# Kernel tuning notes

Hardware: AMD Instinct MI355X
Metric: run time of the kernel (lower is better)

## Reference

```python
import jax, jax.numpy as jnp
import numpy as np

STATE_DIM = 1024
ACTION_DIM = 512
TASK_DIM = 64
EMBED = 64
HID = 128
B = 256


def setup_inputs() -> dict:
    key = jax.random.key(0)
    ks = jax.random.split(key, 24)
    s = 0.02
    inp = {
        "obs": jax.random.normal(ks[0], (B, STATE_DIM), dtype=jnp.float32),
        "task_label": jax.random.normal(ks[1], (B, TASK_DIM), dtype=jnp.float32),
        "action": jax.random.randint(ks[2], (B,), 0, ACTION_DIM, dtype=jnp.int64 if jax.config.jax_enable_x64 else jnp.int32),
        # task encoder: Linear(64,64) ReLU Linear(64,64) ReLU
        "we1": jax.random.normal(ks[3], (TASK_DIM, EMBED)) * s,
        "be1": jnp.zeros((EMBED,), jnp.float32),
        "we2": jax.random.normal(ks[4], (EMBED, EMBED)) * s,
        "be2": jnp.zeros((EMBED,), jnp.float32),
        # h_action net_W: Linear(64,128) ReLU Linear(128, 512*1024)
        "aw1": jax.random.normal(ks[5], (EMBED, HID)) * s,
        "aw1b": jnp.zeros((HID,), jnp.float32),
        "aw2": jax.random.normal(ks[6], (HID, ACTION_DIM * STATE_DIM)) * s,
        "aw2b": jnp.zeros((ACTION_DIM * STATE_DIM,), jnp.float32),
        # h_action net_b: Linear(64,128) ReLU Linear(128, 512)
        "ab1": jax.random.normal(ks[7], (EMBED, HID)) * s,
        "ab1b": jnp.zeros((HID,), jnp.float32),
        "ab2": jax.random.normal(ks[8], (HID, ACTION_DIM)) * s,
        "ab2b": jnp.zeros((ACTION_DIM,), jnp.float32),
        # h_critic net_W: Linear(64,128) ReLU Linear(128, 1*1024)
        "cw1": jax.random.normal(ks[9], (EMBED, HID)) * s,
        "cw1b": jnp.zeros((HID,), jnp.float32),
        "cw2": jax.random.normal(ks[10], (HID, 1 * STATE_DIM)) * s,
        "cw2b": jnp.zeros((STATE_DIM,), jnp.float32),
        # h_critic net_b: Linear(64,128) ReLU Linear(128, 1)
        "cb1": jax.random.normal(ks[11], (EMBED, HID)) * s,
        "cb1b": jnp.zeros((HID,), jnp.float32),
        "cb2": jax.random.normal(ks[12], (HID, 1)) * s,
        "cb2b": jnp.zeros((1,), jnp.float32),
    }
    return inp


def reference(obs, task_label, action, we1, be1, we2, be2,
              aw1, aw1b, aw2, aw2b, ab1, ab1b, ab2, ab2b,
              cw1, cw1b, cw2, cw2b, cb1, cb1b, cb2, cb2b):
    relu = jax.nn.relu
    b = obs.shape[0]
    # DummyBody: phi = phi_a = phi_v = obs
    # task encoder -> z [B, EMBED]
    z = relu(relu(task_label @ we1 + be1) @ we2 + be2)
    # hypernet-generated actor head: W [B, A, S], b [B, A]
    Wa = (relu(z @ aw1 + aw1b) @ aw2 + aw2b).reshape(b, ACTION_DIM, STATE_DIM)
    ba = relu(z @ ab1 + ab1b) @ ab2 + ab2b
    # hypernet-generated critic head: W [B, 1, S], b [B, 1]
    Wv = (relu(z @ cw1 + cw1b) @ cw2 + cw2b).reshape(b, 1, STATE_DIM)
    bv = relu(z @ cb1 + cb1b) @ cb2 + cb2b
    # bmm apply (torch.bmm(W, phi.unsqueeze(-1)).squeeze(-1) + b)
    logits = jnp.einsum('boi,bi->bo', Wa, obs) + ba
    v = jnp.einsum('boi,bi->bo', Wv, obs) + bv
    logp = jax.nn.log_softmax(logits, axis=-1)
    log_prob = jnp.take_along_axis(logp, action[:, None].astype(jnp.int32), axis=-1)  # [B,1]
    entropy = -jnp.sum(jnp.exp(logp) * logp, axis=-1, keepdims=True)  # [B,1]
    return logits, action, log_prob, entropy, v
```

## Files before the change

kernel.cpp:

```cpp
#include <hip/hip_runtime.h>
#include <hip/hip_bf16.h>

#define B_SZ 256
#define SDIM 1024
#define ADIM 512

#define BK 128
#define KSPLIT 2
#define KHALF (SDIM / KSPLIT)
#define NCHUNK (KHALF / BK)
#define ROWS 80
#define PADB 136
#define NSLOT 10

typedef __attribute__((ext_vector_type(8))) short bf16x8;
typedef __attribute__((ext_vector_type(4))) float f32x4;

__device__ __forceinline__ unsigned short f2bf(float x) {
  union { float f; unsigned u; } v; v.f = x;
  unsigned r = v.u + 0x7FFFu + ((v.u >> 16) & 1u);
  return (unsigned short)(r >> 16);
}

__global__ __launch_bounds__(128) void kprep(
    const float* __restrict__ obs,
    const float* __restrict__ task, const int* __restrict__ action,
    const float* __restrict__ we1, const float* __restrict__ be1,
    const float* __restrict__ we2, const float* __restrict__ be2,
    const float* __restrict__ aw1, const float* __restrict__ aw1b,
    const float* __restrict__ ab1, const float* __restrict__ ab1b,
    const float* __restrict__ ab2, const float* __restrict__ ab2b,
    const float* __restrict__ cw1, const float* __restrict__ cw1b,
    const float* __restrict__ cb1, const float* __restrict__ cb1b,
    const float* __restrict__ cb2, const float* __restrict__ cb2b,
    float* __restrict__ ws_ha, float* __restrict__ ws_hc,
    unsigned short* __restrict__ ws_obs,
    float* __restrict__ out)
{
  const int b = blockIdx.x, t = threadIdx.x;
  __shared__ float s_task[64], s_t1[64], s_z[64], s_hb[128], s_red[128];

  {
    const float4* orow = (const float4*)(obs + (size_t)b * SDIM);
    ushort4* wrow = (ushort4*)(ws_obs + (size_t)b * SDIM);
#pragma unroll
    for (int i = 0; i < 2; ++i) {
      const int idx = t + i * 128;
      float4 v = orow[idx];
      ushort4 u;
      u.x = f2bf(v.x); u.y = f2bf(v.y); u.z = f2bf(v.z); u.w = f2bf(v.w);
      wrow[idx] = u;
    }
  }

  if (t < 64) s_task[t] = task[b * 64 + t];
  __syncthreads();
  if (t < 64) {
    float a = be1[t];
    for (int e = 0; e < 64; ++e) a += s_task[e] * we1[e * 64 + t];
    s_t1[t] = fmaxf(a, 0.0f);
  }
  __syncthreads();
  if (t < 64) {
    float a = be2[t];
    for (int e = 0; e < 64; ++e) a += s_t1[e] * we2[e * 64 + t];
    s_z[t] = fmaxf(a, 0.0f);
  }
  __syncthreads();
  {
    float a1 = aw1b[t], a2 = ab1b[t], a3 = cw1b[t], a4 = cb1b[t];
    for (int e = 0; e < 64; ++e) {
      const float zv = s_z[e];
      a1 += zv * aw1[e * 128 + t];
      a2 += zv * ab1[e * 128 + t];
      a3 += zv * cw1[e * 128 + t];
      a4 += zv * cb1[e * 128 + t];
    }
    ws_ha[b * 128 + t] = fmaxf(a1, 0.0f);
    s_hb[t] = fmaxf(a2, 0.0f);
    ws_hc[b * 128 + t] = fmaxf(a3, 0.0f);
    s_red[t] = fmaxf(a4, 0.0f) * cb2[t];
  }
  __syncthreads();
  for (int o = t; o < ADIM; o += 128) {
    float a = ab2b[o];
    for (int h = 0; h < 128; ++h) a += s_hb[h] * ab2[h * ADIM + o];
    out[b * ADIM + o] = a;
  }
  for (int s = 64; s > 0; s >>= 1) {
    __syncthreads();
    if (t < s) s_red[t] += s_red[t + s];
  }
  if (t == 0) {
    out[131840 + b] = s_red[0] + cb2b[0];
    out[131072 + b] = (float)action[b];
  }
}

__global__ __launch_bounds__(256, 2) void khyper(
    const unsigned short* __restrict__ ws_obs,
    const float* __restrict__ aw2, const float* __restrict__ aw2b,
    const float* __restrict__ cw2, const float* __restrict__ cw2b,
    const float* __restrict__ ws_ha, const float* __restrict__ ws_hc,
    float* __restrict__ d_out)
{
  __shared__ unsigned short B_lds[ROWS * PADB];
  __shared__ float logits_buf[B_SZ];

  const int tid = threadIdx.x;
  const int blk = blockIdx.x;
  const int kh   = blk & 1;
  const int half = (blk >> 1) & 1;
  const int col  = blk >> 2;
  const bool critic = (col == ADIM);
  const float* haW = critic ? ws_hc : ws_ha;
  const float* Wbase = critic ? cw2 : (aw2 + (size_t)col * SDIM);
  const size_t wstride = critic ? (size_t)SDIM : (size_t)ADIM * SDIM;
  const float* Bbias = critic ? cw2b : (aw2b + (size_t)col * SDIM);
  const int kbase = kh * KHALF;

  const int lr0 = tid >> 5;
  const int c4  = tid & 31;
  const int g0  = half * ROWS + lr0;
  const float* src0 = Wbase + (size_t)g0 * wstride + c4 * 4 + kbase;
  const size_t off8 = (size_t)8 * wstride;
  const float* biassrc = Bbias + c4 * 4 + kbase;
  const int soff0 = lr0 * PADB + c4 * 4;

  const int lane = tid & 63;
  const int wv = tid >> 6;
  const int mbase = wv * 64;
  const int lrow = lane & 15;
  const int lk8 = (lane >> 4) * 8;

  const unsigned short* pA[4];
#pragma unroll
  for (int mf = 0; mf < 4; ++mf)
    pA[mf] = ws_obs + (size_t)(mbase + mf * 16 + lrow) * SDIM + kbase + lk8;

  f32x4 acc[4][5];
#pragma unroll
  for (int mf = 0; mf < 4; ++mf)
#pragma unroll
    for (int nf = 0; nf < 5; ++nf) acc[mf][nf] = (f32x4)(0.0f);

  float4 sreg[NSLOT];

  auto LOAD = [&](int c) {
    const int k0 = c * BK;
#pragma unroll
    for (int i = 0; i < NSLOT; ++i) {
      const int g = g0 + 8 * i;
      float4 v; v.x = 0.f; v.y = 0.f; v.z = 0.f; v.w = 0.f;
      if (g < 128)       v = *(const float4*)(src0 + (size_t)i * off8 + k0);
      else if (g == 128) v = *(const float4*)(biassrc + k0);
      sreg[i] = v;
    }
  };

  auto WRITE = [&]() {
#pragma unroll
    for (int i = 0; i < NSLOT; ++i) {
      ushort4 p;
      p.x = f2bf(sreg[i].x); p.y = f2bf(sreg[i].y);
      p.z = f2bf(sreg[i].z); p.w = f2bf(sreg[i].w);
      *(ushort4*)(&B_lds[soff0 + i * 8 * PADB]) = p;
    }
  };

  auto COMPUTE = [&](int c) {
    const int kg = c * BK;
#pragma unroll
    for (int kk = 0; kk < BK / 32; ++kk) {
      bf16x8 af[4];
#pragma unroll
      for (int mf = 0; mf < 4; ++mf)
        af[mf] = *(const bf16x8*)(pA[mf] + kg + kk * 32);
      bf16x8 bfr[5];
#pragma unroll
      for (int nf = 0; nf < 5; ++nf)
        bfr[nf] = *(const bf16x8*)(&B_lds[(nf * 16 + lrow) * PADB + kk * 32 + lk8]);
#pragma unroll
      for (int mf = 0; mf < 4; ++mf)
#pragma unroll
        for (int nf = 0; nf < 5; ++nf)
          acc[mf][nf] = __builtin_amdgcn_mfma_f32_16x16x32_bf16(af[mf], bfr[nf], acc[mf][nf], 0, 0, 0);
    }
  };

  const int rot = blk & 3;
  LOAD(rot);
#pragma unroll 1
  for (int c = 0; c < NCHUNK; ++c) {
    const int ce = (c + rot) & 3;
    WRITE();
    asm volatile("s_waitcnt lgkmcnt(0)" ::: "memory");
    __builtin_amdgcn_sched_barrier(0);
    __builtin_amdgcn_s_barrier();
    if (c + 1 < NCHUNK) LOAD((c + 1 + rot) & 3);
    COMPUTE(ce);
    __builtin_amdgcn_sched_barrier(0);
    __builtin_amdgcn_s_barrier();
  }

  if (tid < B_SZ) logits_buf[tid] = 0.0f;
  __syncthreads();

  float val[4][4];
#pragma unroll
  for (int mf = 0; mf < 4; ++mf)
#pragma unroll
    for (int r = 0; r < 4; ++r) val[mf][r] = 0.0f;

#pragma unroll
  for (int nf = 0; nf < 5; ++nf) {
    const int hidx = half * ROWS + nf * 16 + lrow;
    if (hidx < 128) {
#pragma unroll
      for (int mf = 0; mf < 4; ++mf) {
        const int m0 = mbase + mf * 16 + ((lane >> 4) << 2);
#pragma unroll
        for (int r = 0; r < 4; ++r)
          val[mf][r] += haW[(m0 + r) * 128 + hidx] * acc[mf][nf][r];
      }
    } else if (hidx == 128) {
#pragma unroll
      for (int mf = 0; mf < 4; ++mf)
#pragma unroll
        for (int r = 0; r < 4; ++r) val[mf][r] += acc[mf][nf][r];
    }
  }

#pragma unroll
  for (int mf = 0; mf < 4; ++mf)
#pragma unroll
    for (int r = 0; r < 4; ++r) {
      float v = val[mf][r];
      v += __shfl_xor(v, 1, 64);
      v += __shfl_xor(v, 2, 64);
      v += __shfl_xor(v, 4, 64);
      v += __shfl_xor(v, 8, 64);
      val[mf][r] = v;
    }
  if ((lane & 15) == 0) {
#pragma unroll
    for (int mf = 0; mf < 4; ++mf)
#pragma unroll
      for (int r = 0; r < 4; ++r)
        atomicAdd(&logits_buf[mbase + mf * 16 + ((lane >> 4) << 2) + r], val[mf][r]);
  }
  __syncthreads();

  if (tid < B_SZ) {
    if (!critic) atomicAdd(&d_out[(size_t)tid * ADIM + col], logits_buf[tid]);
    else         atomicAdd(&d_out[131840 + tid], logits_buf[tid]);
  }
}

__global__ __launch_bounds__(256) void kfinal(const int* __restrict__ action,
                                              float* __restrict__ d_out)
{
  const int b = blockIdx.x, t = threadIdx.x;
  const float* lrow = d_out + (size_t)b * ADIM;
  __shared__ float sM[4], sS[4], sT[4];

  const float x0 = lrow[t], x1 = lrow[t + 256];
  float m = fmaxf(x0, x1);
#pragma unroll
  for (int s = 1; s < 64; s <<= 1) m = fmaxf(m, __shfl_xor(m, s, 64));
  const int wv = t >> 6, ln = t & 63;
  if (ln == 0) sM[wv] = m;
  __syncthreads();
  m = fmaxf(fmaxf(sM[0], sM[1]), fmaxf(sM[2], sM[3]));

  const float d0 = x0 - m, d1 = x1 - m;
  const float e0 = expf(d0), e1 = expf(d1);
  float s1 = e0 + e1;
  float s2 = e0 * d0 + e1 * d1;
#pragma unroll
  for (int s = 1; s < 64; s <<= 1) {
    s1 += __shfl_xor(s1, s, 64);
    s2 += __shfl_xor(s2, s, 64);
  }
  if (ln == 0) { sS[wv] = s1; sT[wv] = s2; }
  __syncthreads();
  if (t == 0) {
    const float S = sS[0] + sS[1] + sS[2] + sS[3];
    const float T = sT[0] + sT[1] + sT[2] + sT[3];
    const float lnS = logf(S);
    const int a = action[b];
    d_out[131328 + b] = (lrow[a] - m) - lnS;
    d_out[131584 + b] = lnS - T / S;
  }
}

extern "C" void kernel_launch(void* const* d_in, const int* in_sizes, int n_in,
                              void* d_out_v, int out_size, void* d_ws, size_t ws_size,
                              hipStream_t stream) {
  const float* obs   = (const float*)d_in[0];
  const float* task  = (const float*)d_in[1];
  const int*   action= (const int*)  d_in[2];
  const float* we1   = (const float*)d_in[3];
  const float* be1   = (const float*)d_in[4];
  const float* we2   = (const float*)d_in[5];
  const float* be2   = (const float*)d_in[6];
  const float* aw1   = (const float*)d_in[7];
  const float* aw1b  = (const float*)d_in[8];
  const float* aw2   = (const float*)d_in[9];
  const float* aw2b  = (const float*)d_in[10];
  const float* ab1   = (const float*)d_in[11];
  const float* ab1b  = (const float*)d_in[12];
  const float* ab2   = (const float*)d_in[13];
  const float* ab2b  = (const float*)d_in[14];
  const float* cw1   = (const float*)d_in[15];
  const float* cw1b  = (const float*)d_in[16];
  const float* cw2   = (const float*)d_in[17];
  const float* cw2b  = (const float*)d_in[18];
  const float* cb1   = (const float*)d_in[19];
  const float* cb1b  = (const float*)d_in[20];
  const float* cb2   = (const float*)d_in[21];
  const float* cb2b  = (const float*)d_in[22];
  float* out = (float*)d_out_v;
  float* ws_ha = (float*)d_ws;
  float* ws_hc = ws_ha + 256 * 128;
  unsigned short* ws_obs = (unsigned short*)(ws_hc + 256 * 128);

  kprep<<<256, 128, 0, stream>>>(obs, task, action, we1, be1, we2, be2, aw1, aw1b,
                                 ab1, ab1b, ab2, ab2b, cw1, cw1b, cb1, cb1b,
                                 cb2, cb2b, ws_ha, ws_hc, ws_obs, out);
  khyper<<<513 * 4, 256, 0, stream>>>(ws_obs, aw2, aw2b, cw2, cw2b, ws_ha, ws_hc, out);
  kfinal<<<256, 256, 0, stream>>>(action, out);
}
```

Before: 166.6 us.

## Restructure hypernet GEMM to tile over output/hidden with full-batch MFMA per block

Replaces the per-column, K-split hypernet kernel with 552 blocks of 512 threads. Each block streams 16-output by 128-k weight tiles for 8 hidden units and multiplies them against all 256 batch rows. It scales each tile's result by the hidden activation and accumulates in registers, with double-buffered swizzled LDS. The critic bias term cw2b·obs moves into the prep kernel, so the hyper kernel no longer carries a bias row. This aims to cut redundant obs reloads, the shared-memory reduction and atomic traffic. In exchange, each block has few loads in flight and a barrier every step, and 16 hidden groups contend on the output atomics.

```diff
diff --git a/kernel.cpp b/kernel.cpp
--- a/kernel.cpp
+++ b/kernel.cpp
@@ -5,13 +5,8 @@
 #define SDIM 1024
 #define ADIM 512
 
-#define BK 128
-#define KSPLIT 2
-#define KHALF (SDIM / KSPLIT)
-#define NCHUNK (KHALF / BK)
-#define ROWS 80
-#define PADB 136
-#define NSLOT 10
+#define BKC 128
+#define NKC (SDIM / BKC)
 
 typedef __attribute__((ext_vector_type(8))) short bf16x8;
 typedef __attribute__((ext_vector_type(4))) float f32x4;
@@ -33,6 +28,7 @@
     const float* __restrict__ cw1, const float* __restrict__ cw1b,
     const float* __restrict__ cb1, const float* __restrict__ cb1b,
     const float* __restrict__ cb2, const float* __restrict__ cb2b,
+    const float* __restrict__ cw2b,
     float* __restrict__ ws_ha, float* __restrict__ ws_hc,
     unsigned short* __restrict__ ws_obs,
     float* __restrict__ out)
@@ -40,13 +36,17 @@
   const int b = blockIdx.x, t = threadIdx.x;
   __shared__ float s_task[64], s_t1[64], s_z[64], s_hb[128], s_red[128];
 
+  float dotc = 0.0f;
   {
     const float4* orow = (const float4*)(obs + (size_t)b * SDIM);
+    const float4* crow = (const float4*)cw2b;
     ushort4* wrow = (ushort4*)(ws_obs + (size_t)b * SDIM);
 #pragma unroll
     for (int i = 0; i < 2; ++i) {
       const int idx = t + i * 128;
       float4 v = orow[idx];
+      float4 w = crow[idx];
+      dotc += v.x * w.x + v.y * w.y + v.z * w.z + v.w * w.w;
       ushort4 u;
       u.x = f2bf(v.x); u.y = f2bf(v.y); u.z = f2bf(v.z); u.w = f2bf(v.w);
       wrow[idx] = u;
@@ -79,7 +79,7 @@
     ws_ha[b * 128 + t] = fmaxf(a1, 0.0f);
     s_hb[t] = fmaxf(a2, 0.0f);
     ws_hc[b * 128 + t] = fmaxf(a3, 0.0f);
-    s_red[t] = fmaxf(a4, 0.0f) * cb2[t];
+    s_red[t] = fmaxf(a4, 0.0f) * cb2[t] + dotc;
   }
   __syncthreads();
   for (int o = t; o < ADIM; o += 128) {
@@ -97,163 +97,142 @@
   }
 }
 
-__global__ __launch_bounds__(256, 2) void khyper(
+__global__ __launch_bounds__(512, 4) void khyper(
     const unsigned short* __restrict__ ws_obs,
     const float* __restrict__ aw2, const float* __restrict__ aw2b,
-    const float* __restrict__ cw2, const float* __restrict__ cw2b,
+    const float* __restrict__ cw2,
     const float* __restrict__ ws_ha, const float* __restrict__ ws_hc,
     float* __restrict__ d_out)
 {
-  __shared__ unsigned short B_lds[ROWS * PADB];
-  __shared__ float logits_buf[B_SZ];
+  __shared__ unsigned short Wl[2][16 * BKC];
 
   const int tid = threadIdx.x;
   const int blk = blockIdx.x;
-  const int kh   = blk & 1;
-  const int half = (blk >> 1) & 1;
-  const int col  = blk >> 2;
-  const bool critic = (col == ADIM);
-  const float* haW = critic ? ws_hc : ws_ha;
-  const float* Wbase = critic ? cw2 : (aw2 + (size_t)col * SDIM);
-  const size_t wstride = critic ? (size_t)SDIM : (size_t)ADIM * SDIM;
-  const float* Bbias = critic ? cw2b : (aw2b + (size_t)col * SDIM);
-  const int kbase = kh * KHALF;
-
-  const int lr0 = tid >> 5;
-  const int c4  = tid & 31;
-  const int g0  = half * ROWS + lr0;
-  const float* src0 = Wbase + (size_t)g0 * wstride + c4 * 4 + kbase;
-  const size_t off8 = (size_t)8 * wstride;
-  const float* biassrc = Bbias + c4 * 4 + kbase;
-  const int soff0 = lr0 * PADB + c4 * 4;
+
+  int wtype, o0 = 0, h0 = 0, hcount;
+  const float* Wbase;
+  size_t hstride = 0;
+  if (blk < 512) {
+    wtype = 0; o0 = (blk & 31) * 16; h0 = (blk >> 5) * 8; hcount = 8;
+    Wbase = aw2 + ((size_t)h0 * ADIM + o0) * SDIM;
+    hstride = (size_t)ADIM * SDIM;
+  } else if (blk < 544) {
+    wtype = 1; o0 = (blk - 512) * 16; hcount = 1;
+    Wbase = aw2b + (size_t)o0 * SDIM;
+  } else {
+    wtype = 2; hcount = 1;
+    Wbase = cw2 + (size_t)(blk - 544) * 16 * SDIM;
+  }
+  const int steps = NKC * hcount;
+
+  const int sr = tid >> 5;
+  const int sc = tid & 31;
+  const float* wsrc = Wbase + (size_t)sr * SDIM + sc * 4;
+  const int wldsb = ((sr * 256 + sc * 8) ^ ((sr & 7) << 4));
 
   const int lane = tid & 63;
   const int wv = tid >> 6;
-  const int mbase = wv * 64;
   const int lrow = lane & 15;
-  const int lk8 = (lane >> 4) * 8;
-
-  const unsigned short* pA[4];
-#pragma unroll
-  for (int mf = 0; mf < 4; ++mf)
-    pA[mf] = ws_obs + (size_t)(mbase + mf * 16 + lrow) * SDIM + kbase + lk8;
-
-  f32x4 acc[4][5];
-#pragma unroll
-  for (int mf = 0; mf < 4; ++mf)
-#pragma unroll
-    for (int nf = 0; nf < 5; ++nf) acc[mf][nf] = (f32x4)(0.0f);
-
-  float4 sreg[NSLOT];
-
-  auto LOAD = [&](int c) {
-    const int k0 = c * BK;
-#pragma unroll
-    for (int i = 0; i < NSLOT; ++i) {
-      const int g = g0 + 8 * i;
-      float4 v; v.x = 0.f; v.y = 0.f; v.z = 0.f; v.w = 0.f;
-      if (g < 128)       v = *(const float4*)(src0 + (size_t)i * off8 + k0);
-      else if (g == 128) v = *(const float4*)(biassrc + k0);
-      sreg[i] = v;
-    }
+  const int grp = lane >> 4;
+
+  const int b0 = wv * 32 + lrow;
+  const int b1 = wv * 32 + 16 + lrow;
+
+  int ardb[4];
+#pragma unroll
+  for (int ks = 0; ks < 4; ++ks)
+    ardb[ks] = ((lrow * 256 + ks * 64 + grp * 16) ^ ((lrow & 7) << 4));
+
+  f32x4 acc0 = {0.f, 0.f, 0.f, 0.f}, acc1 = {0.f, 0.f, 0.f, 0.f};
+  bf16x8 ob0[4], ob1[4];
+
+  auto LOADW = [&](int t) -> float4 {
+    const int kcn = (hcount == 8) ? (t >> 3) : t;
+    const int hn  = (hcount == 8) ? (t & 7) : 0;
+    return *(const float4*)(wsrc + (size_t)hn * hstride + kcn * BKC);
   };
-
-  auto WRITE = [&]() {
-#pragma unroll
-    for (int i = 0; i < NSLOT; ++i) {
-      ushort4 p;
-      p.x = f2bf(sreg[i].x); p.y = f2bf(sreg[i].y);
-      p.z = f2bf(sreg[i].z); p.w = f2bf(sreg[i].w);
-      *(ushort4*)(&B_lds[soff0 + i * 8 * PADB]) = p;
-    }
+  auto WRITEW = [&](int buf, float4 v) {
+    ushort4 p;
+    p.x = f2bf(v.x); p.y = f2bf(v.y); p.z = f2bf(v.z); p.w = f2bf(v.w);
+    *(ushort4*)((char*)(&Wl[buf][0]) + wldsb) = p;
   };
-
-  auto COMPUTE = [&](int c) {
-    const int kg = c * BK;
-#pragma unroll
-    for (int kk = 0; kk < BK / 32; ++kk) {
-      bf16x8 af[4];
-#pragma unroll
-      for (int mf = 0; mf < 4; ++mf)
-        af[mf] = *(const bf16x8*)(pA[mf] + kg + kk * 32);
-      bf16x8 bfr[5];
-#pragma unroll
-      for (int nf = 0; nf < 5; ++nf)
-        bfr[nf] = *(const bf16x8*)(&B_lds[(nf * 16 + lrow) * PADB + kk * 32 + lk8]);
-#pragma unroll
-      for (int mf = 0; mf < 4; ++mf)
-#pragma unroll
-        for (int nf = 0; nf < 5; ++nf)
-          acc[mf][nf] = __builtin_amdgcn_mfma_f32_16x16x32_bf16(af[mf], bfr[nf], acc[mf][nf], 0, 0, 0);
+  auto PRELOAD = [&](int kc) {
+    const unsigned short* ob = ws_obs + kc * BKC + grp * 8;
+#pragma unroll
+    for (int ks = 0; ks < 4; ++ks) {
+      ob0[ks] = *(const bf16x8*)(ob + (size_t)b0 * SDIM + ks * 32);
+      ob1[ks] = *(const bf16x8*)(ob + (size_t)b1 * SDIM + ks * 32);
     }
   };
-
-  const int rot = blk & 3;
-  LOAD(rot);
+  auto STEP = [&](int buf, int h) {
+    const char* base = (const char*)(&Wl[buf][0]);
+    f32x4 t0 = {0.f, 0.f, 0.f, 0.f}, t1 = {0.f, 0.f, 0.f, 0.f};
+#pragma unroll
+    for (int ks = 0; ks < 4; ++ks) {
+      bf16x8 af = *(const bf16x8*)(base + ardb[ks]);
+      t0 = __builtin_amdgcn_mfma_f32_16x16x32_bf16(af, ob0[ks], t0, 0, 0, 0);
+      t1 = __builtin_amdgcn_mfma_f32_16x16x32_bf16(af, ob1[ks], t1, 0, 0, 0);
+    }
+    if (wtype == 0) {
+      const float w0 = ws_ha[(size_t)b0 * 128 + h0 + h];
+      const float w1 = ws_ha[(size_t)b1 * 128 + h0 + h];
+#pragma unroll
+      for (int r = 0; r < 4; ++r) { acc0[r] += w0 * t0[r]; acc1[r] += w1 * t1[r]; }
+    } else {
+#pragma unroll
+      for (int r = 0; r < 4; ++r) { acc0[r] += t0[r]; acc1[r] += t1[r]; }
+    }
+  };
+
+  float4 sregA = LOADW(0);
+  float4 sregB = LOADW(1);
+  WRITEW(0, sregA);
+  asm volatile("s_waitcnt lgkmcnt(0)" ::: "memory");
+  __builtin_amdgcn_s_barrier();
+
 #pragma unroll 1
-  for (int c = 0; c < NCHUNK; ++c) {
-    const int ce = (c + rot) & 3;
-    WRITE();
+  for (int s = 0; s < steps; s += 2) {
+    const int kcE = (hcount == 8) ? (s >> 3) : s;
+    const int hE  = (hcount == 8) ? (s & 7) : 0;
+    if (hE == 0) PRELOAD(kcE);
+    if (s + 2 < steps) sregA = LOADW(s + 2);
+    STEP(0, hE);
+    WRITEW(1, sregB);
     asm volatile("s_waitcnt lgkmcnt(0)" ::: "memory");
     __builtin_amdgcn_sched_barrier(0);
     __builtin_amdgcn_s_barrier();
-    if (c + 1 < NCHUNK) LOAD((c + 1 + rot) & 3);
-    COMPUTE(ce);
+    const int kcO = (hcount == 8) ? ((s + 1) >> 3) : (s + 1);
+    const int hO  = (hcount == 8) ? ((s + 1) & 7) : 0;
+    if (hO == 0 && hcount == 1) PRELOAD(kcO);
+    if (s + 3 < steps) sregB = LOADW(s + 3);
+    STEP(1, hO);
+    if (s + 2 < steps) WRITEW(0, sregA);
+    asm volatile("s_waitcnt lgkmcnt(0)" ::: "memory");
     __builtin_amdgcn_sched_barrier(0);
     __builtin_amdgcn_s_barrier();
   }
 
-  if (tid < B_SZ) logits_buf[tid] = 0.0f;
-  __syncthreads();
-
-  float val[4][4];
-#pragma unroll
-  for (int mf = 0; mf < 4; ++mf)
-#pragma unroll
-    for (int r = 0; r < 4; ++r) val[mf][r] = 0.0f;
-
-#pragma unroll
-  for (int nf = 0; nf < 5; ++nf) {
-    const int hidx = half * ROWS + nf * 16 + lrow;
-    if (hidx < 128) {
-#pragma unroll
-      for (int mf = 0; mf < 4; ++mf) {
-        const int m0 = mbase + mf * 16 + ((lane >> 4) << 2);
-#pragma unroll
-        for (int r = 0; r < 4; ++r)
-          val[mf][r] += haW[(m0 + r) * 128 + hidx] * acc[mf][nf][r];
-      }
-    } else if (hidx == 128) {
-#pragma unroll
-      for (int mf = 0; mf < 4; ++mf)
-#pragma unroll
-        for (int r = 0; r < 4; ++r) val[mf][r] += acc[mf][nf][r];
-    }
-  }
-
-#pragma unroll
-  for (int mf = 0; mf < 4; ++mf)
+  if (wtype != 2) {
+    const int ob = o0 + grp * 4;
 #pragma unroll
     for (int r = 0; r < 4; ++r) {
-      float v = val[mf][r];
-      v += __shfl_xor(v, 1, 64);
-      v += __shfl_xor(v, 2, 64);
-      v += __shfl_xor(v, 4, 64);
-      v += __shfl_xor(v, 8, 64);
-      val[mf][r] = v;
-    }
-  if ((lane & 15) == 0) {
-#pragma unroll
-    for (int mf = 0; mf < 4; ++mf)
-#pragma unroll
-      for (int r = 0; r < 4; ++r)
-        atomicAdd(&logits_buf[mbase + mf * 16 + ((lane >> 4) << 2) + r], val[mf][r]);
-  }
-  __syncthreads();
-
-  if (tid < B_SZ) {
-    if (!critic) atomicAdd(&d_out[(size_t)tid * ADIM + col], logits_buf[tid]);
-    else         atomicAdd(&d_out[131840 + tid], logits_buf[tid]);
+      atomicAdd(&d_out[(size_t)b0 * ADIM + ob + r], acc0[r]);
+      atomicAdd(&d_out[(size_t)b1 * ADIM + ob + r], acc1[r]);
+    }
+  } else {
+    const int hb = (blk - 544) * 16 + grp * 4;
+    float v0 = 0.f, v1 = 0.f;
+#pragma unroll
+    for (int r = 0; r < 4; ++r) {
+      v0 += ws_hc[(size_t)b0 * 128 + hb + r] * acc0[r];
+      v1 += ws_hc[(size_t)b1 * 128 + hb + r] * acc1[r];
+    }
+    v0 += __shfl_xor(v0, 16, 64); v0 += __shfl_xor(v0, 32, 64);
+    v1 += __shfl_xor(v1, 16, 64); v1 += __shfl_xor(v1, 32, 64);
+    if (grp == 0) {
+      atomicAdd(&d_out[131840 + b0], v0);
+      atomicAdd(&d_out[131840 + b1], v1);
+    }
   }
 }
 
@@ -327,7 +306,7 @@
 
   kprep<<<256, 128, 0, stream>>>(obs, task, action, we1, be1, we2, be2, aw1, aw1b,
                                  ab1, ab1b, ab2, ab2b, cw1, cw1b, cb1, cb1b,
-                                 cb2, cb2b, ws_ha, ws_hc, ws_obs, out);
-  khyper<<<513 * 4, 256, 0, stream>>>(ws_obs, aw2, aw2b, cw2, cw2b, ws_ha, ws_hc, out);
+                                 cb2, cb2b, cw2b, ws_ha, ws_hc, ws_obs, out);
+  khyper<<<552, 512, 0, stream>>>(ws_obs, aw2, aw2b, cw2, ws_ha, ws_hc, out);
   kfinal<<<256, 256, 0, stream>>>(action, out);
 }
```

After: 167.0 us. Within noise of the previous version (+0.3%).
